# Kernel tuning notes

Measured on AMD Instinct MI355X. Metric: run time of the kernel, lower is better.

## Reference

```python
import jax, jax.numpy as jnp
import numpy as np
from jax import lax

B, N, S, K, C = 8, 4096, 1024, 64, 64
RADIUS = 0.2
MLP = [64, 128, 256]
INT_MAX = jnp.iinfo(jnp.int32).max

_batched_gather = jax.vmap(lambda a, i: a[i])  # (N,D),(S,K)->(S,K,D)


def setup_inputs() -> dict:
    key = jax.random.key(0)
    ks = jax.random.split(key, 6)
    xyz = jax.random.uniform(ks[0], (B, N, 3), dtype=jnp.float32)
    points = jax.random.normal(ks[1], (B, N, C), dtype=jnp.float32)
    fps_inds = jax.random.randint(ks[2], (B, S), 0, N, dtype=jnp.int32)
    c_in = [3 + C] + MLP[:-1]
    w0 = jax.random.normal(ks[3], (c_in[0], MLP[0]), dtype=jnp.float32) * 0.1
    w1 = jax.random.normal(ks[4], (c_in[1], MLP[1]), dtype=jnp.float32) * 0.1
    w2 = jax.random.normal(ks[5], (c_in[2], MLP[2]), dtype=jnp.float32) * 0.1
    return {"xyz": xyz, "points": points, "fps_inds": fps_inds,
            "w0": w0, "w1": w1, "w2": w2}


def _query_ball_point(radius, nsample, xyz, new_xyz):
    # dists: (B, S, N)
    dists = jnp.linalg.norm(new_xyz[:, :, None, :] - xyz[:, None, :, :], axis=-1)
    # nsample nearest neighbors (ascending distance), like argsort[:, :, :nsample]
    neg_d, idx = lax.top_k(-dists, nsample)            # (B,S,K)
    valid = (-neg_d) < radius                          # prefix mask (dists ascending)
    idx_m = jnp.where(valid, idx, INT_MAX)
    sidx = jnp.sort(idx_m, axis=-1)
    # invalid slots -> first (smallest) valid index
    return jnp.where(valid, sidx, sidx[:, :, :1])


def reference(xyz, points, fps_inds, w0, w1, w2):
    new_xyz = _batched_gather(xyz, fps_inds)                       # (B,S,3)
    idx = _query_ball_point(RADIUS, K, xyz, new_xyz)               # (B,S,K)
    grouped_xyz = _batched_gather(xyz, idx) - new_xyz[:, :, None]  # (B,S,K,3)
    grouped_pts = _batched_gather(points, idx)                     # (B,S,K,C)
    feat = jnp.concatenate([grouped_xyz, grouped_pts], axis=-1)    # (B,S,K,3+C)
    for w in (w0, w1, w2):  # 1x1 conv == channel matmul, then relu
        feat = jax.nn.relu(jnp.einsum('bskc,cf->bskf', feat, w))
    new_points = jnp.max(feat, axis=2)                             # (B,S,F)
    return new_xyz, new_points
```

## Files before the change

### kernel.cpp

```cpp
#include <hip/hip_runtime.h>

#define NB 8
#define NN 4096
#define NS 1024
#define NC 64
#define OUT_PTS_OFF (NB*NS*3)
#define CAP 512
#define RB 0.2f
#define QPB 8

typedef __attribute__((ext_vector_type(8))) short bf16x8;
typedef __attribute__((ext_vector_type(4))) float f32x4;

static __device__ __forceinline__ short f2bf(float f){
  unsigned u = __float_as_uint(f);
  unsigned r = (u + 0x7FFFu + ((u>>16)&1u)) >> 16;
  return (short)r;
}
static __device__ __forceinline__ float bf2f(short s){
  return __uint_as_float(((unsigned)(unsigned short)s) << 16);
}
static __device__ __forceinline__ unsigned cvtpk(float a, float b){
  unsigned r;
  asm("v_cvt_pk_bf16_f32 %0, %1, %2" : "=v"(r) : "v"(a), "v"(b));
  return r;
}

#define WS_PX1_SH   1048576
#define WS_WF_SH    3145728

__global__ __launch_bounds__(256) void prep_weights(
    const float* __restrict__ w0, const float* __restrict__ w1,
    const float* __restrict__ w2, short* __restrict__ ws)
{
  int e = blockIdx.x*256 + threadIdx.x;
  if (e >= 47104) return;
  float v = 0.f;
  if (e < 6144) {
    int j=e&7, l=(e>>3)&63, nt=(e>>9)&3, kt=e>>11;
    int k = kt*32 + ((l>>4)<<3) + j, n = nt*16 + (l&15);
    if (k < 64) v = w0[(3+k)*64 + n];
    else if (k < 67) v = w0[(k-64)*64 + n];
  } else if (e < 14336) {
    int e2=e-6144;
    int j=e2&7, l=(e2>>3)&63, nt=(e2>>9)&7, kt=e2>>12;
    int k = kt*32 + ((l>>4)<<3) + j, n = nt*16 + (l&15);
    v = w1[k*128 + n];
  } else {
    int e3=e-14336;
    int j=e3&7, l=(e3>>3)&63, nt=(e3>>9)&15, kt=e3>>13;
    int k = (kt*2 + (j&1))*16 + ((l>>4)<<2) + (j>>1);
    v = w2[k*256 + nt*16 + (l&15)];
  }
  ws[e] = f2bf(v);
}

__global__ __launch_bounds__(256) void px1_kernel(
    const float* __restrict__ xyz, const float* __restrict__ points,
    const short* __restrict__ wsb, short* __restrict__ px1)
{
  const int tid = threadIdx.x;
  const int w = tid>>6, l = tid&63, lr = l&15, grp = l>>4;
  const int rowbase = blockIdx.x*64 + w*16;
  const int row = rowbase + lr;
  const float* prow = points + (size_t)row*NC;
  const float* xr   = xyz + (size_t)row*3;

  bf16x8 a0, a1, a2;
  {
    float4 u0 = *(const float4*)(prow + grp*8);
    float4 u1 = *(const float4*)(prow + grp*8 + 4);
    float4 u2 = *(const float4*)(prow + 32 + grp*8);
    float4 u3 = *(const float4*)(prow + 32 + grp*8 + 4);
    a0 = (bf16x8){f2bf(u0.x),f2bf(u0.y),f2bf(u0.z),f2bf(u0.w),f2bf(u1.x),f2bf(u1.y),f2bf(u1.z),f2bf(u1.w)};
    a1 = (bf16x8){f2bf(u2.x),f2bf(u2.y),f2bf(u2.z),f2bf(u2.w),f2bf(u3.x),f2bf(u3.y),f2bf(u3.z),f2bf(u3.w)};
    short e0=0,e1=0,e2v=0;
    if (grp==0) { e0=f2bf(xr[0]); e1=f2bf(xr[1]); e2v=f2bf(xr[2]); }
    a2 = (bf16x8){e0,e1,e2v,0,0,0,0,0};
  }
  f32x4 zero4 = {0.f,0.f,0.f,0.f};
  #pragma unroll
  for (int nt=0; nt<4; ++nt) {
    f32x4 acc = zero4;
    bf16x8 b0 = *(const bf16x8*)(wsb + (((0*4+nt)*64 + l)<<3));
    bf16x8 b1 = *(const bf16x8*)(wsb + (((1*4+nt)*64 + l)<<3));
    bf16x8 b2 = *(const bf16x8*)(wsb + (((2*4+nt)*64 + l)<<3));
    acc = __builtin_amdgcn_mfma_f32_16x16x32_bf16(a0, b0, acc, 0,0,0);
    acc = __builtin_amdgcn_mfma_f32_16x16x32_bf16(a1, b1, acc, 0,0,0);
    acc = __builtin_amdgcn_mfma_f32_16x16x32_bf16(a2, b2, acc, 0,0,0);
    #pragma unroll
    for (int i=0;i<4;++i)
      px1[(size_t)(rowbase + grp*4 + i)*64 + nt*16 + lr] = f2bf(acc[i]);
  }
}

__global__ __launch_bounds__(256) void grid_build(
    const float* __restrict__ xyz, float4* __restrict__ gxyz, int* __restrict__ cstart)
{
  __shared__ int hist[125];
  __shared__ int base[125];
  const int b = blockIdx.x, tid = threadIdx.x;
  const float* xb = xyz + (size_t)b*NN*3;

  if (tid < 125) hist[tid] = 0;
  __syncthreads();

  float xs[16], ys[16], zs[16]; int cl[16];
  {
    const float4* xv = (const float4*)(xb + tid*48);
    #pragma unroll
    for (int g=0; g<4; ++g) {
      float4 v0 = xv[g*3], v1 = xv[g*3+1], v2 = xv[g*3+2];
      xs[g*4+0]=v0.x; xs[g*4+1]=v0.w; xs[g*4+2]=v1.z; xs[g*4+3]=v2.y;
      ys[g*4+0]=v0.y; ys[g*4+1]=v1.x; ys[g*4+2]=v1.w; ys[g*4+3]=v2.z;
      zs[g*4+0]=v0.z; zs[g*4+1]=v1.y; zs[g*4+2]=v2.x; zs[g*4+3]=v2.w;
    }
  }
  #pragma unroll
  for (int r=0; r<16; ++r) {
    int cx = min(4, (int)(xs[r]*5.0f));
    int cy = min(4, (int)(ys[r]*5.0f));
    int cz = min(4, (int)(zs[r]*5.0f));
    cl[r] = (cz*5+cy)*5+cx;
    atomicAdd(&hist[cl[r]], 1);
  }
  __syncthreads();
  if (tid == 0) {
    int acc = 0;
    for (int c=0; c<125; ++c) { base[c]=acc; cstart[b*128+c]=acc; acc+=hist[c]; }
    cstart[b*128+125] = NN;
  }
  __syncthreads();
  #pragma unroll
  for (int r=0; r<16; ++r) {
    int slot = atomicAdd(&base[cl[r]], 1);
    gxyz[b*NN + slot] = make_float4(xs[r], ys[r], zs[r], __int_as_float(tid*16+r));
  }
}

__global__ __launch_bounds__(256) void select_kernel(
    const float* __restrict__ xyz, const int* __restrict__ fps_inds,
    const float4* __restrict__ gxyz, const int* __restrict__ cstart,
    unsigned short* __restrict__ gsidx, float* __restrict__ out)
{
  __shared__ unsigned int cand_d[CAP];
  __shared__ int cand_i[CAP];
  __shared__ int scell[126];
  __shared__ int seg_s[27], seg_b[27], seg_e[27];
  __shared__ int tmp64[64];
  __shared__ int cnt_sh, T_sh;

  const int q = blockIdx.x, b = q >> 10, tid = threadIdx.x;
  const float* xb = xyz + (size_t)b*NN*3;
  const int fps = fps_inds[q];
  const float qx = xb[fps*3+0], qy = xb[fps*3+1], qz = xb[fps*3+2];
  if (tid < 3) out[q*3+tid] = xb[fps*3+tid];
  if (tid < 126) scell[tid] = cstart[b*128+tid];
  if (tid == 0) cnt_sh = 0;
  __syncthreads();

  if (tid < 32) {
    const int cx = min(4, (int)(qx*5.0f));
    const int cy = min(4, (int)(qy*5.0f));
    const int cz = min(4, (int)(qz*5.0f));
    int len = 0, s = 0;
    if (tid < 27) {
      int ncx = cx + tid%3 - 1, ncy = cy + (tid/3)%3 - 1, ncz = cz + tid/9 - 1;
      if (ncx>=0 && ncx<5 && ncy>=0 && ncy<5 && ncz>=0 && ncz<5) {
        float lox = ncx*0.2f - 1e-5f, hix = lox + 0.2f + 2e-5f;
        float loy = ncy*0.2f - 1e-5f, hiy = loy + 0.2f + 2e-5f;
        float loz = ncz*0.2f - 1e-5f, hiz = loz + 0.2f + 2e-5f;
        float dx = fmaxf(0.f, fmaxf(lox-qx, qx-hix));
        float dy = fmaxf(0.f, fmaxf(loy-qy, qy-hiy));
        float dz = fmaxf(0.f, fmaxf(loz-qz, qz-hiz));
        if (fmaf(dx,dx, fmaf(dy,dy, dz*dz)) <= 0.0402f) {
          int c = (ncz*5+ncy)*5+ncx;
          s = scell[c]; len = scell[c+1] - s;
        }
      }
    }
    int incl = len;
    #pragma unroll
    for (int off=1; off<32; off<<=1) {
      int v = __shfl_up(incl, off, 32);
      if (tid >= off) incl += v;
    }
    if (tid < 27) { seg_s[tid]=s; seg_b[tid]=incl-len; seg_e[tid]=incl; }
    if (tid == 31) T_sh = incl;
  }
  __syncthreads();

  const int T = T_sh;
  const float4* gb = gxyz + b*NN;
  {
    int k = 0;
    for (int t = tid; t < T; t += 256) {
      while (t >= seg_e[k]) ++k;
      float4 p = gb[seg_s[k] + (t - seg_b[k])];
      float fx = qx-p.x, fy = qy-p.y, fz = qz-p.z;
      float ff = fmaf(fx,fx, fmaf(fy,fy, fz*fz));
      if (ff < 0.0402f) {
        float dx=__fsub_rn(qx,p.x), dy=__fsub_rn(qy,p.y), dz=__fsub_rn(qz,p.z);
        float d2=__fadd_rn(__fadd_rn(__fmul_rn(dx,dx),__fmul_rn(dy,dy)),__fmul_rn(dz,dz));
        float d = __fsqrt_rn(d2);
        if (d < RB) {
          int pos = atomicAdd(&cnt_sh, 1);
          if (pos < CAP) { cand_d[pos] = __float_as_uint(d); cand_i[pos] = __float_as_int(p.w); }
        }
      }
    }
  }
  __syncthreads();
  int cnt = cnt_sh; if (cnt > CAP) cnt = CAP;

  if (cnt > 64) {
    for (int j=tid; j<cnt; j+=256) {
      unsigned dj = cand_d[j]; int ij = cand_i[j]; int rk = 0;
      for (int i=0; i<cnt; ++i) {
        unsigned di = cand_d[i];
        rk += (int)((di<dj) | ((di==dj) & (cand_i[i]<ij)));
      }
      if (rk < 64) tmp64[rk] = ij;
    }
    __syncthreads();
    if (tid < 64) {
      int v = tmp64[tid]; int p = 0;
      #pragma unroll
      for (int u=0; u<64; ++u) p += (tmp64[u] < v);
      gsidx[q*64 + p] = (unsigned short)v;
    }
  } else {
    if (tid < cnt) {
      int v = cand_i[tid]; int p = 0;
      for (int u=0; u<cnt; ++u) p += (cand_i[u] < v);
      tmp64[p] = v;
    }
    __syncthreads();
    if (tid < 64) gsidx[q*64 + tid] = (unsigned short)tmp64[tid < cnt ? tid : 0];
  }
}

__global__ __launch_bounds__(256,2) void mlp_kernel(
    const float* __restrict__ xyz, const int* __restrict__ fps_inds,
    const float* __restrict__ w0, const short* __restrict__ wsb,
    const short* __restrict__ px1, const unsigned short* __restrict__ gsidx,
    float* __restrict__ out)
{
  __shared__ __align__(16) short w1s[16*64*8];
  __shared__ __align__(16) short h2f[8192];
  __shared__ float q1s[QPB][64];
  __shared__ int sidx[QPB][64];

  const int tid = threadIdx.x;
  const int w = tid>>6, l = tid&63, lr = l&15, grp = l>>4;
  const int q0 = blockIdx.x*QPB;
  const int b = q0 >> 10;
  const float* xb = xyz + (size_t)b*NN*3;

  bf16x8 b3[4][4];
  #pragma unroll
  for (int kt=0; kt<4; ++kt)
    #pragma unroll
    for (int j=0; j<4; ++j)
      b3[kt][j] = *(const bf16x8*)(wsb + 14336 + (((kt*16 + w*4 + j)*64 + l)<<3));

  #pragma unroll
  for (int e = 0; e < 4; ++e) {
    int s = tid + e*256;
    *(bf16x8*)&w1s[s*8] = *(const bf16x8*)(wsb + 6144 + s*8);
  }
  for (int e = tid; e < QPB*64; e += 256) {
    int qq = e>>6, t = e&63;
    int fp = fps_inds[q0+qq];
    sidx[qq][t] = (int)gsidx[(q0+qq)*64 + t];
    q1s[qq][t] = xb[fp*3]*w0[t] + xb[fp*3+1]*w0[64+t] + xb[fp*3+2]*w0[128+t];
  }
  if (tid < QPB*3) {
    int qq = tid/3, c = tid - qq*3;
    int fp = fps_inds[q0+qq];
    out[(q0+qq)*3 + c] = xb[fp*3+c];
  }
  __syncthreads();

  const short* px1b = px1 + (size_t)b*NN*64;
  const int myrow = w*16 + lr;

  bf16x8 v0, v1;
  {
    int idx = sidx[0][myrow];
    v0 = *(const bf16x8*)(px1b + idx*64 + grp*8);
    v1 = *(const bf16x8*)(px1b + idx*64 + 32 + grp*8);
  }

  f32x4 zero4 = {0.f,0.f,0.f,0.f};
  const int uu4 = (lr>>2) << 4;
  const int gg4 = grp << 4;

  for (int qq = 0; qq < QPB; ++qq) {
    if (qq) __syncthreads();

    bf16x8 a20, a21;
    {
      union { unsigned u[4]; bf16x8 v; } ua, ub;
      #pragma unroll
      for (int jp=0; jp<4; ++jp) {
        float x0 = fmaxf(bf2f(v0[2*jp  ]) - q1s[qq][grp*8+2*jp  ], 0.f);
        float x1 = fmaxf(bf2f(v0[2*jp+1]) - q1s[qq][grp*8+2*jp+1], 0.f);
        ua.u[jp] = cvtpk(x0, x1);
        float y0 = fmaxf(bf2f(v1[2*jp  ]) - q1s[qq][32+grp*8+2*jp  ], 0.f);
        float y1 = fmaxf(bf2f(v1[2*jp+1]) - q1s[qq][32+grp*8+2*jp+1], 0.f);
        ub.u[jp] = cvtpk(y0, y1);
      }
      a20 = ua.v; a21 = ub.v;
    }
    if (qq+1 < QPB) {
      int idx = sidx[qq+1][myrow];
      v0 = *(const bf16x8*)(px1b + idx*64 + grp*8);
      v1 = *(const bf16x8*)(px1b + idx*64 + 32 + grp*8);
    }

    #pragma unroll
    for (int ntp=0; ntp<4; ++ntp) {
      f32x4 accA = zero4, accB = zero4;
      bf16x8 bA0 = *(const bf16x8*)&w1s[((0*8 + 2*ntp  )*64 + l)*8];
      bf16x8 bA1 = *(const bf16x8*)&w1s[((1*8 + 2*ntp  )*64 + l)*8];
      bf16x8 bB0 = *(const bf16x8*)&w1s[((0*8 + 2*ntp+1)*64 + l)*8];
      bf16x8 bB1 = *(const bf16x8*)&w1s[((1*8 + 2*ntp+1)*64 + l)*8];
      accA = __builtin_amdgcn_mfma_f32_16x16x32_bf16(a20, bA0, accA, 0,0,0);
      accA = __builtin_amdgcn_mfma_f32_16x16x32_bf16(a21, bA1, accA, 0,0,0);
      accB = __builtin_amdgcn_mfma_f32_16x16x32_bf16(a20, bB0, accB, 0,0,0);
      accB = __builtin_amdgcn_mfma_f32_16x16x32_bf16(a21, bB1, accB, 0,0,0);
      #pragma unroll
      for (int i=0; i<4; ++i) {
        unsigned pv = cvtpk(fmaxf(accA[i],0.f), fmaxf(accB[i],0.f));
        int byteoff = ((((w*4+ntp)*64 + (lr>>2)*16 + grp*4 + i)<<4) + ((lr&3)<<2)) ^ uu4;
        *(unsigned*)((char*)h2f + byteoff) = pv;
      }
    }
    __syncthreads();

    f32x4 acc3[4][4];
    #pragma unroll
    for (int mt=0; mt<4; ++mt)
      #pragma unroll
      for (int j=0; j<4; ++j) acc3[mt][j] = zero4;
    #pragma unroll
    for (int kt=0; kt<4; ++kt)
      #pragma unroll
      for (int mt=0; mt<4; ++mt) {
        int byteoff = ((((mt*4+kt)*64 + l)<<4)) ^ gg4;
        bf16x8 a = *(const bf16x8*)((const char*)h2f + byteoff);
        #pragma unroll
        for (int j=0; j<4; ++j)
          acc3[mt][j] = __builtin_amdgcn_mfma_f32_16x16x32_bf16(a, b3[kt][j], acc3[mt][j], 0,0,0);
      }
    #pragma unroll
    for (int j=0; j<4; ++j) {
      float m = 0.f;
      #pragma unroll
      for (int mt=0; mt<4; ++mt) {
        f32x4 t = acc3[mt][j];
        m = fmaxf(m, fmaxf(fmaxf(t[0],t[1]), fmaxf(t[2],t[3])));
      }
      m = fmaxf(m, __shfl_xor(m, 16, 64));
      m = fmaxf(m, __shfl_xor(m, 32, 64));
      if (grp == 0) out[OUT_PTS_OFF + (q0+qq)*256 + (w*4+j)*16 + lr] = m;
    }
  }
}

extern "C" void kernel_launch(void* const* d_in, const int* in_sizes, int n_in,
                              void* d_out, int out_size, void* d_ws, size_t ws_size,
                              hipStream_t stream) {
  const float* xyz      = (const float*)d_in[0];
  const float* points   = (const float*)d_in[1];
  const int*   fps_inds = (const int*)d_in[2];
  const float* w0       = (const float*)d_in[3];
  const float* w1       = (const float*)d_in[4];
  const float* w2       = (const float*)d_in[5];
  float* out = (float*)d_out;

  unsigned short* gsidx = (unsigned short*)d_ws;
  float4* gxyz  = (float4*)((char*)d_ws + 1048576);
  int*    cstart= (int*)((char*)d_ws + 1572864);
  short*  px1   = (short*)d_ws + WS_PX1_SH;
  short*  wsb   = (short*)d_ws + WS_WF_SH;

  hipLaunchKernelGGL(prep_weights, dim3(184), dim3(256), 0, stream, w0, w1, w2, wsb);
  hipLaunchKernelGGL(grid_build,   dim3(NB),  dim3(256), 0, stream, xyz, gxyz, cstart);
  hipLaunchKernelGGL(px1_kernel,   dim3(512), dim3(256), 0, stream, xyz, points, wsb, px1);
  hipLaunchKernelGGL(select_kernel,dim3(NB*NS), dim3(256), 0, stream,
                     xyz, fps_inds, gxyz, cstart, gsidx, out);
  hipLaunchKernelGGL(mlp_kernel,   dim3(NB*NS/QPB), dim3(256), 0, stream,
                     xyz, fps_inds, w0, wsb, px1, gsidx, out);
}
```

Measured before the change: 108.1 us.

## Fuse ball-query selection into MLP kernel and merge weight prep with grid build

The per-query neighbor selection, previously its own kernel with one block per query, now runs inside the MLP kernel, one query at a time for the block's 8 queries. It reuses the h2f shared buffer as candidate scratch and writes sorted indices straight into shared sidx, so the gsidx global round trip is gone. Weight preprocessing and spatial grid construction are merged into one launch, cutting the launch count from five to three. The final layer now takes its max over each m-tile as soon as that tile finishes, which shrinks the live accumulator set. The trade-off is that selection is serialized within each MLP block, with more barriers and less parallelism than a separate grid of 8192 blocks.

After: 200.1 us. 1.85x slower.

```diff
diff --git a/kernel.cpp b/kernel.cpp
--- a/kernel.cpp
+++ b/kernel.cpp
@@ -29,30 +29,76 @@
 #define WS_PX1_SH   1048576
 #define WS_WF_SH    3145728
 
-__global__ __launch_bounds__(256) void prep_weights(
+__global__ __launch_bounds__(256) void prep_grid(
     const float* __restrict__ w0, const float* __restrict__ w1,
-    const float* __restrict__ w2, short* __restrict__ ws)
+    const float* __restrict__ w2, short* __restrict__ ws,
+    const float* __restrict__ xyz, float4* __restrict__ gxyz,
+    int* __restrict__ cstart)
 {
-  int e = blockIdx.x*256 + threadIdx.x;
-  if (e >= 47104) return;
-  float v = 0.f;
-  if (e < 6144) {
-    int j=e&7, l=(e>>3)&63, nt=(e>>9)&3, kt=e>>11;
-    int k = kt*32 + ((l>>4)<<3) + j, n = nt*16 + (l&15);
-    if (k < 64) v = w0[(3+k)*64 + n];
-    else if (k < 67) v = w0[(k-64)*64 + n];
-  } else if (e < 14336) {
-    int e2=e-6144;
-    int j=e2&7, l=(e2>>3)&63, nt=(e2>>9)&7, kt=e2>>12;
-    int k = kt*32 + ((l>>4)<<3) + j, n = nt*16 + (l&15);
-    v = w1[k*128 + n];
-  } else {
-    int e3=e-14336;
-    int j=e3&7, l=(e3>>3)&63, nt=(e3>>9)&15, kt=e3>>13;
-    int k = (kt*2 + (j&1))*16 + ((l>>4)<<2) + (j>>1);
-    v = w2[k*256 + nt*16 + (l&15)];
-  }
-  ws[e] = f2bf(v);
+  __shared__ int hist[125];
+  __shared__ int base[125];
+  const int tid = threadIdx.x;
+
+  if (blockIdx.x < 184) {
+    int e = blockIdx.x*256 + tid;
+    if (e >= 47104) return;
+    float v = 0.f;
+    if (e < 6144) {
+      int j=e&7, l=(e>>3)&63, nt=(e>>9)&3, kt=e>>11;
+      int k = kt*32 + ((l>>4)<<3) + j, n = nt*16 + (l&15);
+      if (k < 64) v = w0[(3+k)*64 + n];
+      else if (k < 67) v = w0[(k-64)*64 + n];
+    } else if (e < 14336) {
+      int e2=e-6144;
+      int j=e2&7, l=(e2>>3)&63, nt=(e2>>9)&7, kt=e2>>12;
+      int k = kt*32 + ((l>>4)<<3) + j, n = nt*16 + (l&15);
+      v = w1[k*128 + n];
+    } else {
+      int e3=e-14336;
+      int j=e3&7, l=(e3>>3)&63, nt=(e3>>9)&15, kt=e3>>13;
+      int k = (kt*2 + (j&1))*16 + ((l>>4)<<2) + (j>>1);
+      v = w2[k*256 + nt*16 + (l&15)];
+    }
+    ws[e] = f2bf(v);
+    return;
+  }
+
+  const int b = blockIdx.x - 184;
+  const float* xb = xyz + (size_t)b*NN*3;
+  if (tid < 125) hist[tid] = 0;
+  __syncthreads();
+
+  float xs[16], ys[16], zs[16]; int cl[16];
+  {
+    const float4* xv = (const float4*)(xb + tid*48);
+    #pragma unroll
+    for (int g=0; g<4; ++g) {
+      float4 v0 = xv[g*3], v1 = xv[g*3+1], v2 = xv[g*3+2];
+      xs[g*4+0]=v0.x; xs[g*4+1]=v0.w; xs[g*4+2]=v1.z; xs[g*4+3]=v2.y;
+      ys[g*4+0]=v0.y; ys[g*4+1]=v1.x; ys[g*4+2]=v1.w; ys[g*4+3]=v2.z;
+      zs[g*4+0]=v0.z; zs[g*4+1]=v1.y; zs[g*4+2]=v2.x; zs[g*4+3]=v2.w;
+    }
+  }
+  #pragma unroll
+  for (int r=0; r<16; ++r) {
+    int cx = min(4, (int)(xs[r]*5.0f));
+    int cy = min(4, (int)(ys[r]*5.0f));
+    int cz = min(4, (int)(zs[r]*5.0f));
+    cl[r] = (cz*5+cy)*5+cx;
+    atomicAdd(&hist[cl[r]], 1);
+  }
+  __syncthreads();
+  if (tid == 0) {
+    int acc = 0;
+    for (int c=0; c<125; ++c) { base[c]=acc; cstart[b*128+c]=acc; acc+=hist[c]; }
+    cstart[b*128+125] = NN;
+  }
+  __syncthreads();
+  #pragma unroll
+  for (int r=0; r<16; ++r) {
+    int slot = atomicAdd(&base[cl[r]], 1);
+    gxyz[b*NN + slot] = make_float4(xs[r], ys[r], zs[r], __int_as_float(tid*16+r));
+  }
 }
 
 __global__ __launch_bounds__(256) void px1_kernel(
@@ -94,162 +140,25 @@
   }
 }
 
-__global__ __launch_bounds__(256) void grid_build(
-    const float* __restrict__ xyz, float4* __restrict__ gxyz, int* __restrict__ cstart)
-{
-  __shared__ int hist[125];
-  __shared__ int base[125];
-  const int b = blockIdx.x, tid = threadIdx.x;
-  const float* xb = xyz + (size_t)b*NN*3;
-
-  if (tid < 125) hist[tid] = 0;
-  __syncthreads();
-
-  float xs[16], ys[16], zs[16]; int cl[16];
-  {
-    const float4* xv = (const float4*)(xb + tid*48);
-    #pragma unroll
-    for (int g=0; g<4; ++g) {
-      float4 v0 = xv[g*3], v1 = xv[g*3+1], v2 = xv[g*3+2];
-      xs[g*4+0]=v0.x; xs[g*4+1]=v0.w; xs[g*4+2]=v1.z; xs[g*4+3]=v2.y;
-      ys[g*4+0]=v0.y; ys[g*4+1]=v1.x; ys[g*4+2]=v1.w; ys[g*4+3]=v2.z;
-      zs[g*4+0]=v0.z; zs[g*4+1]=v1.y; zs[g*4+2]=v2.x; zs[g*4+3]=v2.w;
-    }
-  }
-  #pragma unroll
-  for (int r=0; r<16; ++r) {
-    int cx = min(4, (int)(xs[r]*5.0f));
-    int cy = min(4, (int)(ys[r]*5.0f));
-    int cz = min(4, (int)(zs[r]*5.0f));
-    cl[r] = (cz*5+cy)*5+cx;
-    atomicAdd(&hist[cl[r]], 1);
-  }
-  __syncthreads();
-  if (tid == 0) {
-    int acc = 0;
-    for (int c=0; c<125; ++c) { base[c]=acc; cstart[b*128+c]=acc; acc+=hist[c]; }
-    cstart[b*128+125] = NN;
-  }
-  __syncthreads();
-  #pragma unroll
-  for (int r=0; r<16; ++r) {
-    int slot = atomicAdd(&base[cl[r]], 1);
-    gxyz[b*NN + slot] = make_float4(xs[r], ys[r], zs[r], __int_as_float(tid*16+r));
-  }
-}
-
-__global__ __launch_bounds__(256) void select_kernel(
-    const float* __restrict__ xyz, const int* __restrict__ fps_inds,
-    const float4* __restrict__ gxyz, const int* __restrict__ cstart,
-    unsigned short* __restrict__ gsidx, float* __restrict__ out)
-{
-  __shared__ unsigned int cand_d[CAP];
-  __shared__ int cand_i[CAP];
-  __shared__ int scell[126];
-  __shared__ int seg_s[27], seg_b[27], seg_e[27];
-  __shared__ int tmp64[64];
-  __shared__ int cnt_sh, T_sh;
-
-  const int q = blockIdx.x, b = q >> 10, tid = threadIdx.x;
-  const float* xb = xyz + (size_t)b*NN*3;
-  const int fps = fps_inds[q];
-  const float qx = xb[fps*3+0], qy = xb[fps*3+1], qz = xb[fps*3+2];
-  if (tid < 3) out[q*3+tid] = xb[fps*3+tid];
-  if (tid < 126) scell[tid] = cstart[b*128+tid];
-  if (tid == 0) cnt_sh = 0;
-  __syncthreads();
-
-  if (tid < 32) {
-    const int cx = min(4, (int)(qx*5.0f));
-    const int cy = min(4, (int)(qy*5.0f));
-    const int cz = min(4, (int)(qz*5.0f));
-    int len = 0, s = 0;
-    if (tid < 27) {
-      int ncx = cx + tid%3 - 1, ncy = cy + (tid/3)%3 - 1, ncz = cz + tid/9 - 1;
-      if (ncx>=0 && ncx<5 && ncy>=0 && ncy<5 && ncz>=0 && ncz<5) {
-        float lox = ncx*0.2f - 1e-5f, hix = lox + 0.2f + 2e-5f;
-        float loy = ncy*0.2f - 1e-5f, hiy = loy + 0.2f + 2e-5f;
-        float loz = ncz*0.2f - 1e-5f, hiz = loz + 0.2f + 2e-5f;
-        float dx = fmaxf(0.f, fmaxf(lox-qx, qx-hix));
-        float dy = fmaxf(0.f, fmaxf(loy-qy, qy-hiy));
-        float dz = fmaxf(0.f, fmaxf(loz-qz, qz-hiz));
-        if (fmaf(dx,dx, fmaf(dy,dy, dz*dz)) <= 0.0402f) {
-          int c = (ncz*5+ncy)*5+ncx;
-          s = scell[c]; len = scell[c+1] - s;
-        }
-      }
-    }
-    int incl = len;
-    #pragma unroll
-    for (int off=1; off<32; off<<=1) {
-      int v = __shfl_up(incl, off, 32);
-      if (tid >= off) incl += v;
-    }
-    if (tid < 27) { seg_s[tid]=s; seg_b[tid]=incl-len; seg_e[tid]=incl; }
-    if (tid == 31) T_sh = incl;
-  }
-  __syncthreads();
-
-  const int T = T_sh;
-  const float4* gb = gxyz + b*NN;
-  {
-    int k = 0;
-    for (int t = tid; t < T; t += 256) {
-      while (t >= seg_e[k]) ++k;
-      float4 p = gb[seg_s[k] + (t - seg_b[k])];
-      float fx = qx-p.x, fy = qy-p.y, fz = qz-p.z;
-      float ff = fmaf(fx,fx, fmaf(fy,fy, fz*fz));
-      if (ff < 0.0402f) {
-        float dx=__fsub_rn(qx,p.x), dy=__fsub_rn(qy,p.y), dz=__fsub_rn(qz,p.z);
-        float d2=__fadd_rn(__fadd_rn(__fmul_rn(dx,dx),__fmul_rn(dy,dy)),__fmul_rn(dz,dz));
-        float d = __fsqrt_rn(d2);
-        if (d < RB) {
-          int pos = atomicAdd(&cnt_sh, 1);
-          if (pos < CAP) { cand_d[pos] = __float_as_uint(d); cand_i[pos] = __float_as_int(p.w); }
-        }
-      }
-    }
-  }
-  __syncthreads();
-  int cnt = cnt_sh; if (cnt > CAP) cnt = CAP;
-
-  if (cnt > 64) {
-    for (int j=tid; j<cnt; j+=256) {
-      unsigned dj = cand_d[j]; int ij = cand_i[j]; int rk = 0;
-      for (int i=0; i<cnt; ++i) {
-        unsigned di = cand_d[i];
-        rk += (int)((di<dj) | ((di==dj) & (cand_i[i]<ij)));
-      }
-      if (rk < 64) tmp64[rk] = ij;
-    }
-    __syncthreads();
-    if (tid < 64) {
-      int v = tmp64[tid]; int p = 0;
-      #pragma unroll
-      for (int u=0; u<64; ++u) p += (tmp64[u] < v);
-      gsidx[q*64 + p] = (unsigned short)v;
-    }
-  } else {
-    if (tid < cnt) {
-      int v = cand_i[tid]; int p = 0;
-      for (int u=0; u<cnt; ++u) p += (cand_i[u] < v);
-      tmp64[p] = v;
-    }
-    __syncthreads();
-    if (tid < 64) gsidx[q*64 + tid] = (unsigned short)tmp64[tid < cnt ? tid : 0];
-  }
-}
-
-__global__ __launch_bounds__(256,2) void mlp_kernel(
+__global__ __launch_bounds__(256,2) void select_mlp(
     const float* __restrict__ xyz, const int* __restrict__ fps_inds,
     const float* __restrict__ w0, const short* __restrict__ wsb,
-    const short* __restrict__ px1, const unsigned short* __restrict__ gsidx,
-    float* __restrict__ out)
+    const short* __restrict__ px1, const float4* __restrict__ gxyz,
+    const int* __restrict__ cstart, float* __restrict__ out)
 {
-  __shared__ __align__(16) short w1s[16*64*8];
+  __shared__ __align__(16) short w1s[8192];
   __shared__ __align__(16) short h2f[8192];
   __shared__ float q1s[QPB][64];
   __shared__ int sidx[QPB][64];
+  __shared__ int scell[126];
+  __shared__ int cnt_sh, T_sh;
+
+  unsigned* cand_d = (unsigned*)h2f;
+  int* cand_i = (int*)&h2f[1024];
+  int* tmp64  = (int*)&h2f[2048];
+  int* seg_s  = (int*)&h2f[2240];
+  int* seg_b  = (int*)&h2f[2304];
+  int* seg_e  = (int*)&h2f[2368];
 
   const int tid = threadIdx.x;
   const int w = tid>>6, l = tid&63, lr = l&15, grp = l>>4;
@@ -264,21 +173,102 @@
     for (int j=0; j<4; ++j)
       b3[kt][j] = *(const bf16x8*)(wsb + 14336 + (((kt*16 + w*4 + j)*64 + l)<<3));
 
+  if (tid < 126) scell[tid] = cstart[b*128+tid];
+
+  const float4* gb = gxyz + b*NN;
+  for (int qq = 0; qq < QPB; ++qq) {
+    const int q = q0 + qq;
+    const int fps = fps_inds[q];
+    const float qx = xb[fps*3+0], qy = xb[fps*3+1], qz = xb[fps*3+2];
+    if (tid < 3) out[q*3+tid] = xb[fps*3+tid];
+    if (tid == 0) cnt_sh = 0;
+
+    if (tid < 32) {
+      const int cx = min(4, (int)(qx*5.0f));
+      const int cy = min(4, (int)(qy*5.0f));
+      const int cz = min(4, (int)(qz*5.0f));
+      int len = 0, s = 0;
+      if (tid < 27) {
+        int ncx = cx + tid%3 - 1, ncy = cy + (tid/3)%3 - 1, ncz = cz + tid/9 - 1;
+        if (ncx>=0 && ncx<5 && ncy>=0 && ncy<5 && ncz>=0 && ncz<5) {
+          float lox = ncx*0.2f - 1e-5f, hix = lox + 0.2f + 2e-5f;
+          float loy = ncy*0.2f - 1e-5f, hiy = loy + 0.2f + 2e-5f;
+          float loz = ncz*0.2f - 1e-5f, hiz = loz + 0.2f + 2e-5f;
+          float dx = fmaxf(0.f, fmaxf(lox-qx, qx-hix));
+          float dy = fmaxf(0.f, fmaxf(loy-qy, qy-hiy));
+          float dz = fmaxf(0.f, fmaxf(loz-qz, qz-hiz));
+          if (fmaf(dx,dx, fmaf(dy,dy, dz*dz)) <= 0.0402f) {
+            int c = (ncz*5+ncy)*5+ncx;
+            s = scell[c]; len = scell[c+1] - s;
+          }
+        }
+      }
+      int incl = len;
+      #pragma unroll
+      for (int off=1; off<32; off<<=1) {
+        int v = __shfl_up(incl, off, 32);
+        if (tid >= off) incl += v;
+      }
+      if (tid < 27) { seg_s[tid]=s; seg_b[tid]=incl-len; seg_e[tid]=incl; }
+      if (tid == 31) T_sh = incl;
+    }
+    __syncthreads();
+
+    const int T = T_sh;
+    {
+      int k = 0;
+      for (int t = tid; t < T; t += 256) {
+        while (t >= seg_e[k]) ++k;
+        float4 p = gb[seg_s[k] + (t - seg_b[k])];
+        float fx = qx-p.x, fy = qy-p.y, fz = qz-p.z;
+        float ff = fmaf(fx,fx, fmaf(fy,fy, fz*fz));
+        if (ff < 0.0402f) {
+          float dx=__fsub_rn(qx,p.x), dy=__fsub_rn(qy,p.y), dz=__fsub_rn(qz,p.z);
+          float d2=__fadd_rn(__fadd_rn(__fmul_rn(dx,dx),__fmul_rn(dy,dy)),__fmul_rn(dz,dz));
+          float d = __fsqrt_rn(d2);
+          if (d < RB) {
+            int pos = atomicAdd(&cnt_sh, 1);
+            if (pos < CAP) { cand_d[pos] = __float_as_uint(d); cand_i[pos] = __float_as_int(p.w); }
+          }
+        }
+      }
+    }
+    __syncthreads();
+    int cnt = cnt_sh; if (cnt > CAP) cnt = CAP;
+
+    if (cnt > 64) {
+      for (int j=tid; j<cnt; j+=256) {
+        unsigned dj = cand_d[j]; int ij = cand_i[j]; int rk = 0;
+        for (int i=0; i<cnt; ++i) {
+          unsigned di = cand_d[i];
+          rk += (int)((di<dj) | ((di==dj) & (cand_i[i]<ij)));
+        }
+        if (rk < 64) tmp64[rk] = ij;
+      }
+      __syncthreads();
+      if (tid < 64) {
+        int v = tmp64[tid]; int p = 0;
+        #pragma unroll
+        for (int u=0; u<64; ++u) p += (tmp64[u] < v);
+        sidx[qq][p] = v;
+      }
+    } else {
+      if (tid < cnt) {
+        int v = cand_i[tid]; int p = 0;
+        for (int u=0; u<cnt; ++u) p += (cand_i[u] < v);
+        tmp64[p] = v;
+      }
+      __syncthreads();
+      if (tid < 64) sidx[qq][tid] = tmp64[tid < cnt ? tid : 0];
+    }
+    if (tid < 64) q1s[qq][tid] = qx*w0[tid] + qy*w0[64+tid] + qz*w0[128+tid];
+  }
+  __syncthreads();
+
   #pragma unroll
   for (int e = 0; e < 4; ++e) {
     int s = tid + e*256;
     *(bf16x8*)&w1s[s*8] = *(const bf16x8*)(wsb + 6144 + s*8);
-  }
-  for (int e = tid; e < QPB*64; e += 256) {
-    int qq = e>>6, t = e&63;
-    int fp = fps_inds[q0+qq];
-    sidx[qq][t] = (int)gsidx[(q0+qq)*64 + t];
-    q1s[qq][t] = xb[fp*3]*w0[t] + xb[fp*3+1]*w0[64+t] + xb[fp*3+2]*w0[128+t];
-  }
-  if (tid < QPB*3) {
-    int qq = tid/3, c = tid - qq*3;
-    int fp = fps_inds[q0+qq];
-    out[(q0+qq)*3 + c] = xb[fp*3+c];
   }
   __syncthreads();
 
@@ -339,29 +329,30 @@
     }
     __syncthreads();
 
-    f32x4 acc3[4][4];
-    #pragma unroll
-    for (int mt=0; mt<4; ++mt)
-      #pragma unroll
-      for (int j=0; j<4; ++j) acc3[mt][j] = zero4;
-    #pragma unroll
-    for (int kt=0; kt<4; ++kt)
-      #pragma unroll
-      for (int mt=0; mt<4; ++mt) {
+    float rm[4][4];
+    #pragma unroll
+    for (int j=0;j<4;++j)
+      #pragma unroll
+      for (int i=0;i<4;++i) rm[j][i] = 0.f;
+    #pragma unroll
+    for (int mt=0; mt<4; ++mt) {
+      f32x4 acc[4] = {zero4, zero4, zero4, zero4};
+      #pragma unroll
+      for (int kt=0; kt<4; ++kt) {
         int byteoff = ((((mt*4+kt)*64 + l)<<4)) ^ gg4;
         bf16x8 a = *(const bf16x8*)((const char*)h2f + byteoff);
         #pragma unroll
         for (int j=0; j<4; ++j)
-          acc3[mt][j] = __builtin_amdgcn_mfma_f32_16x16x32_bf16(a, b3[kt][j], acc3[mt][j], 0,0,0);
-      }
+          acc[j] = __builtin_amdgcn_mfma_f32_16x16x32_bf16(a, b3[kt][j], acc[j], 0,0,0);
+      }
+      #pragma unroll
+      for (int j=0; j<4; ++j)
+        #pragma unroll
+        for (int i=0; i<4; ++i) rm[j][i] = fmaxf(rm[j][i], acc[j][i]);
+    }
     #pragma unroll
     for (int j=0; j<4; ++j) {
-      float m = 0.f;
-      #pragma unroll
-      for (int mt=0; mt<4; ++mt) {
-        f32x4 t = acc3[mt][j];
-        m = fmaxf(m, fmaxf(fmaxf(t[0],t[1]), fmaxf(t[2],t[3])));
-      }
+      float m = fmaxf(fmaxf(rm[j][0],rm[j][1]), fmaxf(rm[j][2],rm[j][3]));
       m = fmaxf(m, __shfl_xor(m, 16, 64));
       m = fmaxf(m, __shfl_xor(m, 32, 64));
       if (grp == 0) out[OUT_PTS_OFF + (q0+qq)*256 + (w*4+j)*16 + lr] = m;
@@ -380,17 +371,14 @@
   const float* w2       = (const float*)d_in[5];
   float* out = (float*)d_out;
 
-  unsigned short* gsidx = (unsigned short*)d_ws;
   float4* gxyz  = (float4*)((char*)d_ws + 1048576);
   int*    cstart= (int*)((char*)d_ws + 1572864);
   short*  px1   = (short*)d_ws + WS_PX1_SH;
   short*  wsb   = (short*)d_ws + WS_WF_SH;
 
-  hipLaunchKernelGGL(prep_weights, dim3(184), dim3(256), 0, stream, w0, w1, w2, wsb);
-  hipLaunchKernelGGL(grid_build,   dim3(NB),  dim3(256), 0, stream, xyz, gxyz, cstart);
-  hipLaunchKernelGGL(px1_kernel,   dim3(512), dim3(256), 0, stream, xyz, points, wsb, px1);
-  hipLaunchKernelGGL(select_kernel,dim3(NB*NS), dim3(256), 0, stream,
-                     xyz, fps_inds, gxyz, cstart, gsidx, out);
-  hipLaunchKernelGGL(mlp_kernel,   dim3(NB*NS/QPB), dim3(256), 0, stream,
-                     xyz, fps_inds, w0, wsb, px1, gsidx, out);
-}
+  hipLaunchKernelGGL(prep_grid,  dim3(192), dim3(256), 0, stream,
+                     w0, w1, w2, wsb, xyz, gxyz, cstart);
+  hipLaunchKernelGGL(px1_kernel, dim3(512), dim3(256), 0, stream, xyz, points, wsb, px1);
+  hipLaunchKernelGGL(select_mlp, dim3(NB*NS/QPB), dim3(256), 0, stream,
+                     xyz, fps_inds, w0, wsb, px1, gxyz, cstart, out);
+}
```
